# Performance work log

Hardware: AMD Instinct MI355X
Metric: run time of the kernel (lower is better)

The kernel has to match this reference:

```python
import jax, jax.numpy as jnp
import numpy as np

COORD = 5.0
NOOBJ = 0.5
S = 14
B = 2
C = 20
BATCH = 4096


def setup_inputs() -> dict:
    key = jax.random.key(0)
    k1, k2, k3 = jax.random.split(key, 3)
    inp = jax.random.uniform(k1, (BATCH, S, S, 5 * B + C), dtype=jnp.float32)
    tgt = jax.random.uniform(k2, (BATCH, S, S, 5 * B + C), dtype=jnp.float32)
    # target confidence channels must be exactly 0/1 for the obj test
    conf = (jax.random.uniform(k3, (BATCH, S, S, B)) < 0.2).astype(jnp.float32)
    tgt = tgt.at[..., :B].set(conf)
    return {"input": inp, "target": tgt}


def reference(input, target) -> jnp.ndarray:
    n = input.shape[0]
    conf_p = input[..., :B]                      # [N,S,S,B]
    conf_t = target[..., :B]
    box_p = input[..., B:5 * B].reshape(*input.shape[:-1], B, 4)   # [N,S,S,B,4]
    box_t = target[..., B:5 * B].reshape(*target.shape[:-1], B, 4)
    cls_p = input[..., 5 * B:]                   # [N,S,S,C]
    cls_t = target[..., 5 * B:]

    obj = conf_t == 1.0                          # [N,S,S,B]
    has_obj = jnp.any(obj, axis=-1)              # [N,S,S]
    # first responsible box per cell (the original breaks at first k with obj==1)
    first = obj & (jnp.cumsum(obj.astype(jnp.int32), axis=-1) == 1)  # [N,S,S,B]
    firstf = first.astype(input.dtype)

    sq_xy = jnp.sum((box_p[..., :2] - box_t[..., :2]) ** 2, axis=-1)               # [N,S,S,B]
    sq_wh = jnp.sum((jnp.sqrt(box_p[..., 2:]) - jnp.sqrt(box_t[..., 2:])) ** 2, axis=-1)
    sq_conf = (conf_p - conf_t) ** 2                                               # [N,S,S,B]

    loss_xy = jnp.sum(firstf * sq_xy)
    loss_wh = jnp.sum(firstf * sq_wh)
    loss_objc = jnp.sum(firstf * sq_conf)
    # class loss counted once per cell containing an object
    loss_cls = jnp.sum(has_obj.astype(input.dtype) * jnp.sum((cls_p - cls_t) ** 2, axis=-1))
    # no-object: all B confidences in cells with no responsible box
    noobj_mask = (~has_obj).astype(input.dtype)[..., None]
    loss_noobjc = jnp.sum(noobj_mask * sq_conf)

    total = COORD * (loss_xy + loss_wh) + NOOBJ * loss_noobjc + loss_objc + loss_cls
    return total / n
```

## Files before the change

kernel.cpp:

```cpp
#include <hip/hip_runtime.h>


#define COORD 5.0f
#define NOOBJ 0.5f

#define NCELLS   (4096 * 14 * 14)
#define CPC      128
#define CHB      (CPC * 120)
#define NCHUNKS  (NCELLS / CPC)
#define GRID     512

__device__ __forceinline__ float d2f(float a, float b) { float d = a - b; return d * d; }
__device__ __forceinline__ float sqd(float a, float b) {
    return a + b - 2.0f * sqrtf(a * b);
}

__global__ __launch_bounds__(64) void yolo_loss_kernel(
    const float* __restrict__ inp,
    const float* __restrict__ tgt,
    float* __restrict__ out,
    float inv_n)
{
    __shared__ __align__(16) char smem[2][2][CHB];
    const int lane = threadIdx.x;

    const char* gi0 = (const char*)inp + (size_t)lane * 16;
    const char* gt0 = (const char*)tgt + (size_t)lane * 16;

    auto stage = [&](int b, int c) {
        const char* gi = gi0 + (size_t)c * CHB;
        const char* gt = gt0 + (size_t)c * CHB;
        char* li = &smem[b][0][0];
        char* lt = &smem[b][1][0];
#pragma unroll
        for (int k = 0; k < 15; ++k) {
            __builtin_amdgcn_global_load_lds(
                (const __attribute__((address_space(1))) void*)(gi + k * 1024),
                (__attribute__((address_space(3))) void*)(li + k * 1024), 16, 0, 0);
            __builtin_amdgcn_global_load_lds(
                (const __attribute__((address_space(1))) void*)(gt + k * 1024),
                (__attribute__((address_space(3))) void*)(lt + k * 1024), 16, 0, 0);
        }
    };

    float acc = 0.0f;
    int c = blockIdx.x;
    stage(0, c);
    int buf = 0;

    for (; c < NCHUNKS; c += GRID) {
        const int cn = c + GRID;
        if (cn < NCHUNKS) {
            stage(buf ^ 1, cn);
            asm volatile("s_waitcnt vmcnt(30)" ::: "memory");
        } else {
            asm volatile("s_waitcnt vmcnt(0)" ::: "memory");
        }

        const float4* ia = (const float4*)(&smem[buf][0][0] + lane * 240);
        const float4* ta = (const float4*)(&smem[buf][1][0] + lane * 240);

        float4 I0 = ia[0],  T0 = ta[0];
        float4 I1 = ia[1],  T1 = ta[1];
        float4 I2 = ia[2],  T2 = ta[2];
        float4 I3 = ia[3],  T3 = ta[3];
        float4 I4 = ia[4],  T4 = ta[4];
        float4 I5 = ia[5],  T5 = ta[5];
        float4 I6 = ia[6],  T6 = ta[6];
        float4 I7 = ia[7],  T7 = ta[7];
        float4 I8 = ia[8],  T8 = ta[8];
        float4 I9 = ia[9],  T9 = ta[9];
        float4 I10 = ia[10], T10 = ta[10];
        float4 I11 = ia[11], T11 = ta[11];
        float4 I12 = ia[12], T12 = ta[12];
        float4 I13 = ia[13], T13 = ta[13];
        float4 I14 = ia[14], T14 = ta[14];

        {
            bool o0 = (T0.x == 1.0f), o1 = (T0.y == 1.0f);
            float f0 = o0 ? 1.0f : 0.0f;
            float f1 = (o1 && !o0) ? 1.0f : 0.0f;
            float nf = (o0 || o1) ? 0.0f : 1.0f;
            float h  = 1.0f - nf;
            float s0 = d2f(I0.x, T0.x), s1 = d2f(I0.y, T0.y);
            float xy0 = d2f(I0.z, T0.z) + d2f(I0.w, T0.w);
            float wh0 = sqd(I1.x, T1.x) + sqd(I1.y, T1.y);
            float xy1 = d2f(I1.z, T1.z) + d2f(I1.w, T1.w);
            float wh1 = sqd(I2.x, T2.x) + sqd(I2.y, T2.y);
            float cls = d2f(I2.z, T2.z) + d2f(I2.w, T2.w)
                      + d2f(I3.x, T3.x) + d2f(I3.y, T3.y) + d2f(I3.z, T3.z) + d2f(I3.w, T3.w)
                      + d2f(I4.x, T4.x) + d2f(I4.y, T4.y) + d2f(I4.z, T4.z) + d2f(I4.w, T4.w)
                      + d2f(I5.x, T5.x) + d2f(I5.y, T5.y) + d2f(I5.z, T5.z) + d2f(I5.w, T5.w)
                      + d2f(I6.x, T6.x) + d2f(I6.y, T6.y) + d2f(I6.z, T6.z) + d2f(I6.w, T6.w)
                      + d2f(I7.x, T7.x) + d2f(I7.y, T7.y);
            acc += COORD * (f0 * (xy0 + wh0) + f1 * (xy1 + wh1))
                 + f0 * s0 + f1 * s1
                 + NOOBJ * nf * (s0 + s1)
                 + h * cls;
        }
        {
            bool o0 = (T7.z == 1.0f), o1 = (T7.w == 1.0f);
            float f0 = o0 ? 1.0f : 0.0f;
            float f1 = (o1 && !o0) ? 1.0f : 0.0f;
            float nf = (o0 || o1) ? 0.0f : 1.0f;
            float h  = 1.0f - nf;
            float s0 = d2f(I7.z, T7.z), s1 = d2f(I7.w, T7.w);
            float xy0 = d2f(I8.x, T8.x) + d2f(I8.y, T8.y);
            float wh0 = sqd(I8.z, T8.z) + sqd(I8.w, T8.w);
            float xy1 = d2f(I9.x, T9.x) + d2f(I9.y, T9.y);
            float wh1 = sqd(I9.z, T9.z) + sqd(I9.w, T9.w);
            float cls = d2f(I10.x, T10.x) + d2f(I10.y, T10.y) + d2f(I10.z, T10.z) + d2f(I10.w, T10.w)
                      + d2f(I11.x, T11.x) + d2f(I11.y, T11.y) + d2f(I11.z, T11.z) + d2f(I11.w, T11.w)
                      + d2f(I12.x, T12.x) + d2f(I12.y, T12.y) + d2f(I12.z, T12.z) + d2f(I12.w, T12.w)
                      + d2f(I13.x, T13.x) + d2f(I13.y, T13.y) + d2f(I13.z, T13.z) + d2f(I13.w, T13.w)
                      + d2f(I14.x, T14.x) + d2f(I14.y, T14.y) + d2f(I14.z, T14.z) + d2f(I14.w, T14.w);
            acc += COORD * (f0 * (xy0 + wh0) + f1 * (xy1 + wh1))
                 + f0 * s0 + f1 * s1
                 + NOOBJ * nf * (s0 + s1)
                 + h * cls;
        }

        buf ^= 1;
    }

#pragma unroll
    for (int off = 32; off > 0; off >>= 1)
        acc += __shfl_down(acc, off, 64);
    if (lane == 0) atomicAdd(out, acc * inv_n);
}

extern "C" void kernel_launch(void* const* d_in, const int* in_sizes, int n_in,
                              void* d_out, int out_size, void* d_ws, size_t ws_size,
                              hipStream_t stream) {
    const float* inp = (const float*)d_in[0];
    const float* tgt = (const float*)d_in[1];
    float* out = (float*)d_out;

    hipMemsetAsync(out, 0, sizeof(float), stream);
    yolo_loss_kernel<<<GRID, 64, 0, stream>>>(inp, tgt, out, 1.0f / 4096.0f);
}
```

Measured before the change: 42.41 us.

## Split each cell across two lanes and shrink chunks to raise block count

Chunks shrink from 128 to 32 cells per block and the grid grows from 512 to 2560 blocks, so more waves are resident to hide memory latency. Each cell is now handled by a lane pair: one lane computes the box, confidence and first five class terms, the other the remaining fifteen class terms. The LDS staging is restructured around the 3840-byte chunk, using 16-byte and 4-byte direct-to-LDS loads. In exchange there are many scalar LDS reads at a 15-float stride (bank conflicts), divergent branches within each lane pair, and more atomics at the end.

```diff
diff --git a/kernel.cpp b/kernel.cpp
--- a/kernel.cpp
+++ b/kernel.cpp
@@ -5,10 +5,10 @@
 #define NOOBJ 0.5f
 
 #define NCELLS   (4096 * 14 * 14)
-#define CPC      128
+#define CPC      32
 #define CHB      (CPC * 120)
 #define NCHUNKS  (NCELLS / CPC)
-#define GRID     512
+#define GRID     2560
 
 __device__ __forceinline__ float d2f(float a, float b) { float d = a - b; return d * d; }
 __device__ __forceinline__ float sqd(float a, float b) {
@@ -24,22 +24,28 @@
     __shared__ __align__(16) char smem[2][2][CHB];
     const int lane = threadIdx.x;
 
-    const char* gi0 = (const char*)inp + (size_t)lane * 16;
-    const char* gt0 = (const char*)tgt + (size_t)lane * 16;
-
     auto stage = [&](int b, int c) {
-        const char* gi = gi0 + (size_t)c * CHB;
-        const char* gt = gt0 + (size_t)c * CHB;
+        const char* gi = (const char*)inp + (size_t)c * CHB;
+        const char* gt = (const char*)tgt + (size_t)c * CHB;
         char* li = &smem[b][0][0];
         char* lt = &smem[b][1][0];
 #pragma unroll
-        for (int k = 0; k < 15; ++k) {
+        for (int k = 0; k < 3; ++k) {
             __builtin_amdgcn_global_load_lds(
-                (const __attribute__((address_space(1))) void*)(gi + k * 1024),
+                (const __attribute__((address_space(1))) void*)(gi + k * 1024 + lane * 16),
                 (__attribute__((address_space(3))) void*)(li + k * 1024), 16, 0, 0);
             __builtin_amdgcn_global_load_lds(
-                (const __attribute__((address_space(1))) void*)(gt + k * 1024),
+                (const __attribute__((address_space(1))) void*)(gt + k * 1024 + lane * 16),
                 (__attribute__((address_space(3))) void*)(lt + k * 1024), 16, 0, 0);
+        }
+#pragma unroll
+        for (int k = 0; k < 3; ++k) {
+            __builtin_amdgcn_global_load_lds(
+                (const __attribute__((address_space(1))) void*)(gi + 3072 + k * 256 + lane * 4),
+                (__attribute__((address_space(3))) void*)(li + 3072 + k * 256), 4, 0, 0);
+            __builtin_amdgcn_global_load_lds(
+                (const __attribute__((address_space(1))) void*)(gt + 3072 + k * 256 + lane * 4),
+                (__attribute__((address_space(3))) void*)(lt + 3072 + k * 256), 4, 0, 0);
         }
     };
 
@@ -48,76 +54,50 @@
     stage(0, c);
     int buf = 0;
 
+    const int p = lane >> 1;
+    const int half = lane & 1;
+
     for (; c < NCHUNKS; c += GRID) {
         const int cn = c + GRID;
         if (cn < NCHUNKS) {
             stage(buf ^ 1, cn);
-            asm volatile("s_waitcnt vmcnt(30)" ::: "memory");
+            asm volatile("s_waitcnt vmcnt(12)" ::: "memory");
         } else {
             asm volatile("s_waitcnt vmcnt(0)" ::: "memory");
         }
 
-        const float4* ia = (const float4*)(&smem[buf][0][0] + lane * 240);
-        const float4* ta = (const float4*)(&smem[buf][1][0] + lane * 240);
+        const float* li = (const float*)&smem[buf][0][0];
+        const float* lt = (const float*)&smem[buf][1][0];
+        const float* ip = li + 15 * lane;
+        const float* tp = lt + 15 * lane;
 
-        float4 I0 = ia[0],  T0 = ta[0];
-        float4 I1 = ia[1],  T1 = ta[1];
-        float4 I2 = ia[2],  T2 = ta[2];
-        float4 I3 = ia[3],  T3 = ta[3];
-        float4 I4 = ia[4],  T4 = ta[4];
-        float4 I5 = ia[5],  T5 = ta[5];
-        float4 I6 = ia[6],  T6 = ta[6];
-        float4 I7 = ia[7],  T7 = ta[7];
-        float4 I8 = ia[8],  T8 = ta[8];
-        float4 I9 = ia[9],  T9 = ta[9];
-        float4 I10 = ia[10], T10 = ta[10];
-        float4 I11 = ia[11], T11 = ta[11];
-        float4 I12 = ia[12], T12 = ta[12];
-        float4 I13 = ia[13], T13 = ta[13];
-        float4 I14 = ia[14], T14 = ta[14];
+        float t0 = lt[p * 30];
+        float t1 = lt[p * 30 + 1];
+        bool o0 = (t0 == 1.0f), o1 = (t1 == 1.0f);
+        float f0 = o0 ? 1.0f : 0.0f;
+        float f1 = (o1 && !o0) ? 1.0f : 0.0f;
+        float h  = (o0 || o1) ? 1.0f : 0.0f;
+        float nf = 1.0f - h;
 
-        {
-            bool o0 = (T0.x == 1.0f), o1 = (T0.y == 1.0f);
-            float f0 = o0 ? 1.0f : 0.0f;
-            float f1 = (o1 && !o0) ? 1.0f : 0.0f;
-            float nf = (o0 || o1) ? 0.0f : 1.0f;
-            float h  = 1.0f - nf;
-            float s0 = d2f(I0.x, T0.x), s1 = d2f(I0.y, T0.y);
-            float xy0 = d2f(I0.z, T0.z) + d2f(I0.w, T0.w);
-            float wh0 = sqd(I1.x, T1.x) + sqd(I1.y, T1.y);
-            float xy1 = d2f(I1.z, T1.z) + d2f(I1.w, T1.w);
-            float wh1 = sqd(I2.x, T2.x) + sqd(I2.y, T2.y);
-            float cls = d2f(I2.z, T2.z) + d2f(I2.w, T2.w)
-                      + d2f(I3.x, T3.x) + d2f(I3.y, T3.y) + d2f(I3.z, T3.z) + d2f(I3.w, T3.w)
-                      + d2f(I4.x, T4.x) + d2f(I4.y, T4.y) + d2f(I4.z, T4.z) + d2f(I4.w, T4.w)
-                      + d2f(I5.x, T5.x) + d2f(I5.y, T5.y) + d2f(I5.z, T5.z) + d2f(I5.w, T5.w)
-                      + d2f(I6.x, T6.x) + d2f(I6.y, T6.y) + d2f(I6.z, T6.z) + d2f(I6.w, T6.w)
-                      + d2f(I7.x, T7.x) + d2f(I7.y, T7.y);
+        if (half == 0) {
+            float s0  = d2f(ip[0], tp[0]);
+            float s1  = d2f(ip[1], tp[1]);
+            float xy0 = d2f(ip[2], tp[2]) + d2f(ip[3], tp[3]);
+            float wh0 = sqd(ip[4], tp[4]) + sqd(ip[5], tp[5]);
+            float xy1 = d2f(ip[6], tp[6]) + d2f(ip[7], tp[7]);
+            float wh1 = sqd(ip[8], tp[8]) + sqd(ip[9], tp[9]);
+            float cls = d2f(ip[10], tp[10]) + d2f(ip[11], tp[11]) + d2f(ip[12], tp[12])
+                      + d2f(ip[13], tp[13]) + d2f(ip[14], tp[14]);
             acc += COORD * (f0 * (xy0 + wh0) + f1 * (xy1 + wh1))
                  + f0 * s0 + f1 * s1
                  + NOOBJ * nf * (s0 + s1)
                  + h * cls;
-        }
-        {
-            bool o0 = (T7.z == 1.0f), o1 = (T7.w == 1.0f);
-            float f0 = o0 ? 1.0f : 0.0f;
-            float f1 = (o1 && !o0) ? 1.0f : 0.0f;
-            float nf = (o0 || o1) ? 0.0f : 1.0f;
-            float h  = 1.0f - nf;
-            float s0 = d2f(I7.z, T7.z), s1 = d2f(I7.w, T7.w);
-            float xy0 = d2f(I8.x, T8.x) + d2f(I8.y, T8.y);
-            float wh0 = sqd(I8.z, T8.z) + sqd(I8.w, T8.w);
-            float xy1 = d2f(I9.x, T9.x) + d2f(I9.y, T9.y);
-            float wh1 = sqd(I9.z, T9.z) + sqd(I9.w, T9.w);
-            float cls = d2f(I10.x, T10.x) + d2f(I10.y, T10.y) + d2f(I10.z, T10.z) + d2f(I10.w, T10.w)
-                      + d2f(I11.x, T11.x) + d2f(I11.y, T11.y) + d2f(I11.z, T11.z) + d2f(I11.w, T11.w)
-                      + d2f(I12.x, T12.x) + d2f(I12.y, T12.y) + d2f(I12.z, T12.z) + d2f(I12.w, T12.w)
-                      + d2f(I13.x, T13.x) + d2f(I13.y, T13.y) + d2f(I13.z, T13.z) + d2f(I13.w, T13.w)
-                      + d2f(I14.x, T14.x) + d2f(I14.y, T14.y) + d2f(I14.z, T14.z) + d2f(I14.w, T14.w);
-            acc += COORD * (f0 * (xy0 + wh0) + f1 * (xy1 + wh1))
-                 + f0 * s0 + f1 * s1
-                 + NOOBJ * nf * (s0 + s1)
-                 + h * cls;
+        } else {
+            float cls = 0.0f;
+#pragma unroll
+            for (int j = 0; j < 15; ++j)
+                cls += d2f(ip[j], tp[j]);
+            acc += h * cls;
         }
 
         buf ^= 1;
```

Result: slower. 64.66 us (+52.5%).
